# Kernel tuning notes

Measured on AMD Instinct MI355X. Metric: run time of the kernel, lower is better.

Reference implementation:

```python
import jax, jax.numpy as jnp
import numpy as np

N = 8192          # total genes
B = 16            # number of ragged batch groups (equal-size here: 512 each)
D = 768           # hidden_dim
NEG = -1.0e9      # mask fill value used by the original module


def setup_inputs() -> dict:
    key = jax.random.key(0)
    ks = jax.random.split(key, 10)
    s = 0.02
    inp = {
        "gene_embeddings": jax.random.normal(ks[0], (N, D), dtype=jnp.float32),
        # sorted group ids: 16 contiguous groups of 512 genes
        "batch": (jnp.arange(N) // (N // B)).astype(jnp.int64),
        "Wq": jax.random.normal(ks[1], (D, D), dtype=jnp.float32) * s,
        "bq": jnp.zeros((D,), dtype=jnp.float32),
        "Wk": jax.random.normal(ks[2], (D, D), dtype=jnp.float32) * s,
        "bk": jnp.zeros((D,), dtype=jnp.float32),
        "Wv": jax.random.normal(ks[3], (D, D), dtype=jnp.float32) * s,
        "bv": jnp.zeros((D,), dtype=jnp.float32),
        "Wo": jax.random.normal(ks[4], (D, D), dtype=jnp.float32) * s,
        "bo": jnp.zeros((D,), dtype=jnp.float32),
        "beta": jnp.ones((1,), dtype=jnp.float32) * 0.1,
    }
    return inp


def reference(gene_embeddings, batch, Wq, bq, Wk, bk, Wv, bv, Wo, bo, beta):
    # Single-head attention over full hidden_dim (num_heads unused in original).
    x = gene_embeddings
    q = x @ Wq.T + bq                      # [N, D]
    k = x @ Wk.T + bk
    v = x @ Wv.T + bv
    scale = 1.0 / jnp.sqrt(jnp.asarray(D, dtype=x.dtype))
    scores = (q @ k.T) * scale             # [N, N]
    # block-diagonal group mask + diagonal self-mask (same -1e9 fill as torch code)
    same_group = batch[:, None] == batch[None, :]
    eye = jnp.eye(N, dtype=bool)
    allow = same_group & (~eye)
    scores = jnp.where(allow, scores, NEG)
    weights = jax.nn.softmax(scores, axis=-1)   # dropout in eval mode -> identity
    dyn = weights @ v                       # [N, D]
    dyn = dyn @ Wo.T + bo
    return x + beta * dyn
```

## Files before the change

### kernel.cpp

```cpp
#include <hip/hip_runtime.h>
#include <hip/hip_bf16.h>
#include <cstdint>

using u16 = unsigned short;
using u32 = unsigned int;

typedef __bf16 bf16x8 __attribute__((ext_vector_type(8)));
typedef float  f32x4  __attribute__((ext_vector_type(4)));

__device__ __forceinline__ u32 f2b2(float a, float b) {
    __hip_bfloat162 h = __float22bfloat162_rn(float2{a, b});
    u32 u;
    __builtin_memcpy(&u, &h, 4);
    return u;
}
__device__ __forceinline__ float b2f(u16 b) {
    u32 u = (u32)b << 16;
    float f;
    __builtin_memcpy(&f, &u, 4);
    return f;
}

__device__ __forceinline__ void gload_lds16(const u16* g, u16* l) {
    __builtin_amdgcn_global_load_lds(
        (const __attribute__((address_space(1))) void*)g,
        (__attribute__((address_space(3))) void*)l,
        16, 0, 0);
}

__launch_bounds__(256)
__global__ void pack_kernel(const float* __restrict__ x,
                            const float* __restrict__ Wq,
                            const float* __restrict__ Wk,
                            const float* __restrict__ Wv,
                            const float* __restrict__ Wo,
                            const float* __restrict__ bq,
                            const float* __restrict__ bk,
                            const float* __restrict__ bv,
                            u16* __restrict__ xb,
                            u16* __restrict__ Wqkvb,
                            u16* __restrict__ Wob,
                            float* __restrict__ bqkv)
{
    int c = blockIdx.x * 256 + threadIdx.x;
    long e = (long)c * 8;
    const float* src; u16* dst; long off;
    if (e < 6291456L)      { src = x;  dst = xb;              off = e; }
    else if (e < 6881280L) { src = Wq; dst = Wqkvb;           off = e - 6291456L; }
    else if (e < 7471104L) { src = Wk; dst = Wqkvb + 589824;  off = e - 6881280L; }
    else if (e < 8060928L) { src = Wv; dst = Wqkvb + 1179648; off = e - 7471104L; }
    else                   { src = Wo; dst = Wob;             off = e - 8060928L; }
    float4 v0 = *(const float4*)(src + off);
    float4 v1 = *(const float4*)(src + off + 4);
    uint4 o;
    o.x = f2b2(v0.x, v0.y); o.y = f2b2(v0.z, v0.w);
    o.z = f2b2(v1.x, v1.y); o.w = f2b2(v1.z, v1.w);
    *(uint4*)(dst + off) = o;
    if (c < 768)        bqkv[c] = bq[c];
    else if (c < 1536)  bqkv[c] = bk[c - 768];
    else if (c < 2304)  bqkv[c] = bv[c - 1536];
}

template<int TM, int TN, int MODE>
__device__ __forceinline__ void gemm_body(
        const u16* __restrict__ A, int lda, long sAz,
        const u16* __restrict__ B, int ldb, long sBz,
        void* __restrict__ Cv, int ldc, long sCz,
        int K,
        const float* __restrict__ bias,
        const u16* __restrict__ xres,
        const float* __restrict__ betaPtr,
        float scale,
        u16* __restrict__ vTout)
{
    constexpr int FI = TM / 32;
    constexpr int FJ = TN / 32;
    constexpr int CA = TM / 64;
    constexpr int CB = TN / 64;

    __shared__ u16 As[2][TM * 32];
    __shared__ u16 Bs[2][TN * 32];

    const int tid  = threadIdx.x;
    const int g    = blockIdx.z;
    const u16* Ab = A + (long)g * sAz + (long)blockIdx.y * TM * lda;
    const u16* Bb = B + (long)g * sBz + (long)blockIdx.x * TN * ldb;

    const int wave = tid >> 6, lane = tid & 63;
    const int wm = (wave >> 1) * (TM / 2), wn = (wave & 1) * (TN / 2);
    const int ln15 = lane & 15, lq = lane >> 4;

    f32x4 acc[FI][FJ];
#pragma unroll
    for (int i = 0; i < FI; i++)
#pragma unroll
        for (int j = 0; j < FJ; j++)
            acc[i][j] = (f32x4){0.f, 0.f, 0.f, 0.f};

    const int srow = lane >> 2;
    const int sc   = ((lane & 3) ^ ((lane >> 4) & 3)) * 8;
    const u16* Ag[CA]; const u16* Bg[CB];
    int Al[CA], Bl[CB];
#pragma unroll
    for (int t = 0; t < CA; t++) {
        int c = wave * CA + t;
        Ag[t] = Ab + (long)(c * 16 + srow) * lda + sc;
        Al[t] = c * 512;
    }
#pragma unroll
    for (int t = 0; t < CB; t++) {
        int c = wave * CB + t;
        Bg[t] = Bb + (long)(c * 16 + srow) * ldb + sc;
        Bl[t] = c * 512;
    }

    const int foff = ln15 * 32 + ((lq ^ (ln15 >> 2)) * 8);

    const int nk = K >> 5;

#pragma unroll
    for (int t = 0; t < CA; t++) gload_lds16(Ag[t], &As[0][Al[t]]);
#pragma unroll
    for (int t = 0; t < CB; t++) gload_lds16(Bg[t], &Bs[0][Bl[t]]);

    for (int kt = 0; kt < nk; kt++) {
        const int cur = kt & 1;
        __syncthreads();
        if (kt + 1 < nk) {
            const int k0 = (kt + 1) * 32, nxt = cur ^ 1;
#pragma unroll
            for (int t = 0; t < CA; t++) gload_lds16(Ag[t] + k0, &As[nxt][Al[t]]);
#pragma unroll
            for (int t = 0; t < CB; t++) gload_lds16(Bg[t] + k0, &Bs[nxt][Bl[t]]);
        }

        bf16x8 af[FI], bfr[FJ];
#pragma unroll
        for (int i = 0; i < FI; i++)
            af[i] = *(const bf16x8*)&As[cur][(wm / 16 + i) * 512 + foff];
#pragma unroll
        for (int j = 0; j < FJ; j++)
            bfr[j] = *(const bf16x8*)&Bs[cur][(wn / 16 + j) * 512 + foff];
#pragma unroll
        for (int i = 0; i < FI; i++)
#pragma unroll
            for (int j = 0; j < FJ; j++)
                acc[i][j] = __builtin_amdgcn_mfma_f32_16x16x32_bf16(af[i], bfr[j], acc[i][j], 0, 0, 0);
    }

    const int baseRow = blockIdx.y * TM + wm;
    const int baseCol = blockIdx.x * TN + wn;

    if constexpr (MODE == 0) {
        if (baseCol < 1536) {
            u16* C = (u16*)Cv;
#pragma unroll
            for (int i = 0; i < FI; i++)
#pragma unroll
                for (int j = 0; j < FJ; j++) {
                    int col = baseCol + j * 16 + ln15;
                    float bb = bias[col];
                    u32 p01 = f2b2(acc[i][j][0] + bb, acc[i][j][1] + bb);
                    u32 p23 = f2b2(acc[i][j][2] + bb, acc[i][j][3] + bb);
                    long r0 = (long)(baseRow + i * 16 + lq * 4) * ldc + col;
                    C[r0]           = (u16)p01;
                    C[r0 + ldc]     = (u16)(p01 >> 16);
                    C[r0 + 2 * ldc] = (u16)p23;
                    C[r0 + 3 * ldc] = (u16)(p23 >> 16);
                }
        } else {
#pragma unroll
            for (int i = 0; i < FI; i++)
#pragma unroll
                for (int j = 0; j < FJ; j++) {
                    int col = baseCol + j * 16 + ln15;
                    float bb = bias[col];
                    uint2 o;
                    o.x = f2b2(acc[i][j][0] + bb, acc[i][j][1] + bb);
                    o.y = f2b2(acc[i][j][2] + bb, acc[i][j][3] + bb);
                    *(uint2*)(vTout + (long)(col - 1536) * 8192
                              + baseRow + i * 16 + lq * 4) = o;
                }
        }
    } else if constexpr (MODE == 5) {
        u16* C = (u16*)Cv + (long)g * sCz;
#pragma unroll
        for (int i = 0; i < FI; i++)
#pragma unroll
            for (int j = 0; j < FJ; j++) {
                int col = baseCol + j * 16 + ln15;
                float v[4];
#pragma unroll
                for (int r = 0; r < 4; r++) {
                    int row = baseRow + i * 16 + lq * 4 + r;
                    v[r] = acc[i][j][r] * scale;
                    if (row == col) v[r] = -1.0e9f;
                }
                u32 p01 = f2b2(v[0], v[1]);
                u32 p23 = f2b2(v[2], v[3]);
                long r0 = (long)(baseRow + i * 16 + lq * 4) * ldc + col;
                C[r0]           = (u16)p01;
                C[r0 + ldc]     = (u16)(p01 >> 16);
                C[r0 + 2 * ldc] = (u16)p23;
                C[r0 + 3 * ldc] = (u16)(p23 >> 16);
            }
    } else {
        float* C = (float*)Cv;
        float bet = betaPtr[0];
#pragma unroll
        for (int i = 0; i < FI; i++)
#pragma unroll
            for (int j = 0; j < FJ; j++)
#pragma unroll
                for (int r = 0; r < 4; r++) {
                    int row = baseRow + i * 16 + lq * 4 + r;
                    int col = baseCol + j * 16 + ln15;
                    float v = b2f(xres[(long)row * ldc + col])
                              + bet * (acc[i][j][r] + bias[col]);
                    C[(long)row * ldc + col] = v;
                }
    }
}

__launch_bounds__(256)
__global__ void k_qkv(const u16* A, const u16* B, void* C, const float* bias,
                      u16* vTout)
{
    gemm_body<128, 128, 0>(A, 768, 0, B, 768, 0, C, 1536, 0, 768,
                           bias, nullptr, nullptr, 0.f, vTout);
}
__launch_bounds__(256)
__global__ void k_scores(const u16* A, const u16* B, void* C, float scale)
{
    gemm_body<64, 128, 5>(A, 1536, 512L * 1536, B, 1536, 512L * 1536,
                          C, 512, 512L * 512, 768,
                          nullptr, nullptr, nullptr, scale, nullptr);
}
__launch_bounds__(256)
__global__ void k_out(const u16* A, const u16* B, void* C, const float* bias,
                      const u16* xres, const float* betaPtr)
{
    gemm_body<64, 128, 4>(A, 768, 0, B, 768, 0, C, 768, 0, 768,
                          bias, xres, betaPtr, 0.f, nullptr);
}

__launch_bounds__(256)
__global__ void k_pvfused(const u16* __restrict__ S,
                          const u16* __restrict__ vT,
                          u16* __restrict__ dyn)
{
    __shared__ u16 Pl[32 * 512];
    __shared__ u16 Vs[2][128 * 32];

    const int ct = blockIdx.x, rt = blockIdx.y, g = blockIdx.z;
    const int tid = threadIdx.x;
    const int wave = tid >> 6, lane = tid & 63;
    const int ln15 = lane & 15, lq = lane >> 4;

    const int srow = lane >> 2;
    const int sc   = ((lane & 3) ^ ((lane >> 4) & 3)) * 8;
    const u16* Bg[2]; int Bl[2];
#pragma unroll
    for (int t = 0; t < 2; t++) {
        int c = wave * 2 + t;
        Bg[t] = vT + (long)(ct * 128 + c * 16 + srow) * 8192 + g * 512 + sc;
        Bl[t] = c * 512;
    }
    gload_lds16(Bg[0], &Vs[0][Bl[0]]);
    gload_lds16(Bg[1], &Vs[0][Bl[1]]);

    const int r   = tid >> 3;
    const int seg = tid & 7;
    const u16* Srow = S + (long)g * 262144 + (long)(rt * 32 + r) * 512 + seg * 64;
    float e[64];
    float m = -3.0e38f;
#pragma unroll
    for (int j = 0; j < 8; j++) {
        uint4 q = *(const uint4*)(Srow + j * 8);
        u32 w[4] = {q.x, q.y, q.z, q.w};
#pragma unroll
        for (int h = 0; h < 4; h++) {
            float lo = b2f((u16)w[h]);
            float hi = b2f((u16)(w[h] >> 16));
            e[j * 8 + h * 2]     = lo;
            e[j * 8 + h * 2 + 1] = hi;
            m = fmaxf(m, fmaxf(lo, hi));
        }
    }
    m = fmaxf(m, __shfl_xor(m, 1));
    m = fmaxf(m, __shfl_xor(m, 2));
    m = fmaxf(m, __shfl_xor(m, 4));
    float sum = 0.f;
#pragma unroll
    for (int j = 0; j < 64; j++) { e[j] = __expf(e[j] - m); sum += e[j]; }
    sum += __shfl_xor(sum, 1);
    sum += __shfl_xor(sum, 2);
    sum += __shfl_xor(sum, 4);
    const float inv = 1.0f / sum;
#pragma unroll
    for (int jj = 0; jj < 8; jj++) {
        uint4 o;
        o.x = f2b2(e[jj * 8 + 0] * inv, e[jj * 8 + 1] * inv);
        o.y = f2b2(e[jj * 8 + 2] * inv, e[jj * 8 + 3] * inv);
        o.z = f2b2(e[jj * 8 + 4] * inv, e[jj * 8 + 5] * inv);
        o.w = f2b2(e[jj * 8 + 6] * inv, e[jj * 8 + 7] * inv);
        int c = seg * 8 + jj;
        *(uint4*)&Pl[(r * 64 + (c ^ (r & 7))) * 8] = o;
    }

    const int wm = (wave >> 1) * 16;
    const int wn = (wave & 1) * 64;
    const int foff = ln15 * 32 + ((lq ^ (ln15 >> 2)) * 8);
    const int prow = wm + ln15;

    f32x4 acc[4];
#pragma unroll
    for (int j = 0; j < 4; j++) acc[j] = (f32x4){0.f, 0.f, 0.f, 0.f};

    for (int kt = 0; kt < 16; kt++) {
        const int cur = kt & 1;
        __syncthreads();
        if (kt + 1 < 16) {
            const int k0 = (kt + 1) * 32, nxt = cur ^ 1;
            gload_lds16(Bg[0] + k0, &Vs[nxt][Bl[0]]);
            gload_lds16(Bg[1] + k0, &Vs[nxt][Bl[1]]);
        }
        bf16x8 ap = *(const bf16x8*)&Pl[(prow * 64 + ((kt * 4 + lq) ^ (prow & 7))) * 8];
        bf16x8 bfr[4];
#pragma unroll
        for (int j = 0; j < 4; j++)
            bfr[j] = *(const bf16x8*)&Vs[cur][(wn / 16 + j) * 512 + foff];
#pragma unroll
        for (int j = 0; j < 4; j++)
            acc[j] = __builtin_amdgcn_mfma_f32_16x16x32_bf16(ap, bfr[j], acc[j], 0, 0, 0);
    }

    u16* D = dyn + (long)(g * 512 + rt * 32 + wm + lq * 4) * 768;
#pragma unroll
    for (int j = 0; j < 4; j++) {
        int col = ct * 128 + wn + j * 16 + ln15;
        u32 p01 = f2b2(acc[j][0], acc[j][1]);
        u32 p23 = f2b2(acc[j][2], acc[j][3]);
        D[col]            = (u16)p01;
        D[col + 768]      = (u16)(p01 >> 16);
        D[col + 2 * 768]  = (u16)p23;
        D[col + 3 * 768]  = (u16)(p23 >> 16);
    }
}

extern "C" void kernel_launch(void* const* d_in, const int* in_sizes, int n_in,
                              void* d_out, int out_size, void* d_ws, size_t ws_size,
                              hipStream_t stream)
{
    const float* x    = (const float*)d_in[0];
    const float* Wq   = (const float*)d_in[2];
    const float* bq   = (const float*)d_in[3];
    const float* Wk   = (const float*)d_in[4];
    const float* bk   = (const float*)d_in[5];
    const float* Wv   = (const float*)d_in[6];
    const float* bv   = (const float*)d_in[7];
    const float* Wo   = (const float*)d_in[8];
    const float* bo   = (const float*)d_in[9];
    const float* beta = (const float*)d_in[10];
    float* out = (float*)d_out;

    char* ws = (char*)d_ws;
    u16*   qk    = (u16*)(ws + 0);
    u16*   dyn   = (u16*)(ws + 0);
    u16*   vT    = (u16*)(ws + 25165824);
    u16*   xb    = (u16*)(ws + 37748736);
    u16*   S     = (u16*)(ws + 50331648);
    u16*   Wqkvb = (u16*)(ws + 58720256);
    u16*   Wob   = (u16*)(ws + 62259200);
    float* bqkv  = (float*)(ws + 63438848);

    const float scale = 0.03608439182435161f;

    pack_kernel<<<4224, 256, 0, stream>>>(x, Wq, Wk, Wv, Wo, bq, bk, bv,
                                          xb, Wqkvb, Wob, bqkv);

    k_qkv<<<dim3(18, 64, 1), 256, 0, stream>>>(xb, Wqkvb, (void*)qk, bqkv, vT);

    k_scores<<<dim3(4, 8, 16), 256, 0, stream>>>(qk, qk + 768, (void*)S, scale);

    k_pvfused<<<dim3(6, 16, 16), 256, 0, stream>>>(S, vT, dyn);

    k_out<<<dim3(6, 128, 1), 256, 0, stream>>>(dyn, Wob, (void*)out, bo, xb, beta);
}
```

Measured before the change: 224.0 us.

## Fold output projection into value projection to drop the final GEMM

Precomputes Wo·Wv as a combined matrix and Wo·bv+bo as a combined bias, so the value projection produces already-projected values. The PV kernel then writes the residual output directly, which removes the separate output-projection GEMM over all 8192 rows and the dyn intermediate round trip. In exchange it adds a small 768x768 weight GEMM and a transpose in the pack step. The product weight is rounded to bf16, which slightly changes numerics.

```diff
diff --git a/kernel.cpp b/kernel.cpp
--- a/kernel.cpp
+++ b/kernel.cpp
@@ -37,28 +37,68 @@
                             const float* __restrict__ bq,
                             const float* __restrict__ bk,
                             const float* __restrict__ bv,
+                            const float* __restrict__ bo,
                             u16* __restrict__ xb,
                             u16* __restrict__ Wqkvb,
                             u16* __restrict__ Wob,
-                            float* __restrict__ bqkv)
-{
-    int c = blockIdx.x * 256 + threadIdx.x;
-    long e = (long)c * 8;
-    const float* src; u16* dst; long off;
-    if (e < 6291456L)      { src = x;  dst = xb;              off = e; }
-    else if (e < 6881280L) { src = Wq; dst = Wqkvb;           off = e - 6291456L; }
-    else if (e < 7471104L) { src = Wk; dst = Wqkvb + 589824;  off = e - 6881280L; }
-    else if (e < 8060928L) { src = Wv; dst = Wqkvb + 1179648; off = e - 7471104L; }
-    else                   { src = Wo; dst = Wob;             off = e - 8060928L; }
-    float4 v0 = *(const float4*)(src + off);
-    float4 v1 = *(const float4*)(src + off + 4);
-    uint4 o;
-    o.x = f2b2(v0.x, v0.y); o.y = f2b2(v0.z, v0.w);
-    o.z = f2b2(v1.x, v1.y); o.w = f2b2(v1.z, v1.w);
-    *(uint4*)(dst + off) = o;
-    if (c < 768)        bqkv[c] = bq[c];
-    else if (c < 1536)  bqkv[c] = bk[c - 768];
-    else if (c < 2304)  bqkv[c] = bv[c - 1536];
+                            u16* __restrict__ WvTb,
+                            float* __restrict__ bqk,
+                            float* __restrict__ bvoo)
+{
+    __shared__ u16 tl[64][72];
+    const int b = blockIdx.x, tid = threadIdx.x;
+
+    if (b < 3936) {
+        int c = b * 256 + tid;
+        long e = (long)c * 8;
+        const float* src; u16* dst; long off;
+        if (e < 6291456L)      { src = x;  dst = xb;             off = e; }
+        else if (e < 6881280L) { src = Wq; dst = Wqkvb;          off = e - 6291456L; }
+        else if (e < 7471104L) { src = Wk; dst = Wqkvb + 589824; off = e - 6881280L; }
+        else                   { src = Wo; dst = Wob;            off = e - 7471104L; }
+        float4 v0 = *(const float4*)(src + off);
+        float4 v1 = *(const float4*)(src + off + 4);
+        uint4 o;
+        o.x = f2b2(v0.x, v0.y); o.y = f2b2(v0.z, v0.w);
+        o.z = f2b2(v1.x, v1.y); o.w = f2b2(v1.z, v1.w);
+        *(uint4*)(dst + off) = o;
+        if (c < 768)       bqk[c] = bq[c];
+        else if (c < 1536) bqk[c] = bk[c - 768];
+    } else if (b < 4080) {
+        int t = b - 3936;
+        int tr = t / 12, tc = t % 12;
+        int lr = tid >> 2, lcb = (tid & 3) * 16;
+        const float* src = Wv + (long)(tr * 64 + lr) * 768 + tc * 64 + lcb;
+#pragma unroll
+        for (int q = 0; q < 4; q++) {
+            float4 v = *(const float4*)(src + q * 4);
+            u32 p0 = f2b2(v.x, v.y), p1 = f2b2(v.z, v.w);
+            tl[lr][lcb + q * 4 + 0] = (u16)p0;
+            tl[lr][lcb + q * 4 + 1] = (u16)(p0 >> 16);
+            tl[lr][lcb + q * 4 + 2] = (u16)p1;
+            tl[lr][lcb + q * 4 + 3] = (u16)(p1 >> 16);
+        }
+        __syncthreads();
+        int li = tid >> 2, lkb = (tid & 3) * 16;
+        u16 o[16];
+#pragma unroll
+        for (int j = 0; j < 16; j++) o[j] = tl[lkb + j][li];
+        u16* dst = WvTb + (long)(tc * 64 + li) * 768 + tr * 64 + lkb;
+#pragma unroll
+        for (int j = 0; j < 16; j++) dst[j] = o[j];
+    } else {
+        int wave = tid >> 6, lane = tid & 63;
+        int j = (b - 4080) * 4 + wave;
+        float acc = 0.f;
+#pragma unroll
+        for (int i = 0; i < 12; i++) {
+            int k = i * 64 + lane;
+            acc += Wo[(long)j * 768 + k] * bv[k];
+        }
+#pragma unroll
+        for (int d = 32; d; d >>= 1) acc += __shfl_xor(acc, d);
+        if (lane == 0) bvoo[j] = acc + bo[j];
+    }
 }
 
 template<int TM, int TN, int MODE>
@@ -68,8 +108,6 @@
         void* __restrict__ Cv, int ldc, long sCz,
         int K,
         const float* __restrict__ bias,
-        const u16* __restrict__ xres,
-        const float* __restrict__ betaPtr,
         float scale,
         u16* __restrict__ vTout)
 {
@@ -115,7 +153,6 @@
     }
 
     const int foff = ln15 * 32 + ((lq ^ (ln15 >> 2)) * 8);
-
     const int nk = K >> 5;
 
 #pragma unroll
@@ -174,10 +211,9 @@
 #pragma unroll
                 for (int j = 0; j < FJ; j++) {
                     int col = baseCol + j * 16 + ln15;
-                    float bb = bias[col];
                     uint2 o;
-                    o.x = f2b2(acc[i][j][0] + bb, acc[i][j][1] + bb);
-                    o.y = f2b2(acc[i][j][2] + bb, acc[i][j][3] + bb);
+                    o.x = f2b2(acc[i][j][0], acc[i][j][1]);
+                    o.y = f2b2(acc[i][j][2], acc[i][j][3]);
                     *(uint2*)(vTout + (long)(col - 1536) * 8192
                               + baseRow + i * 16 + lq * 4) = o;
                 }
@@ -205,49 +241,51 @@
                 C[r0 + 3 * ldc] = (u16)(p23 >> 16);
             }
     } else {
-        float* C = (float*)Cv;
-        float bet = betaPtr[0];
+        u16* C = (u16*)Cv;
 #pragma unroll
         for (int i = 0; i < FI; i++)
 #pragma unroll
-            for (int j = 0; j < FJ; j++)
-#pragma unroll
-                for (int r = 0; r < 4; r++) {
-                    int row = baseRow + i * 16 + lq * 4 + r;
-                    int col = baseCol + j * 16 + ln15;
-                    float v = b2f(xres[(long)row * ldc + col])
-                              + bet * (acc[i][j][r] + bias[col]);
-                    C[(long)row * ldc + col] = v;
-                }
-    }
-}
-
+            for (int j = 0; j < FJ; j++) {
+                int col = baseCol + j * 16 + ln15;
+                u32 p01 = f2b2(acc[i][j][0], acc[i][j][1]);
+                u32 p23 = f2b2(acc[i][j][2], acc[i][j][3]);
+                long r0 = (long)(baseRow + i * 16 + lq * 4) * ldc + col;
+                C[r0]           = (u16)p01;
+                C[r0 + ldc]     = (u16)(p01 >> 16);
+                C[r0 + 2 * ldc] = (u16)p23;
+                C[r0 + 3 * ldc] = (u16)(p23 >> 16);
+            }
+    }
+}
+
+__launch_bounds__(256)
+__global__ void k_wvo(const u16* A, const u16* B, void* C)
+{
+    gemm_body<64, 128, 3>(A, 768, 0, B, 768, 0, C, 768, 0, 768,
+                          nullptr, 0.f, nullptr);
+}
 __launch_bounds__(256)
 __global__ void k_qkv(const u16* A, const u16* B, void* C, const float* bias,
                       u16* vTout)
 {
     gemm_body<128, 128, 0>(A, 768, 0, B, 768, 0, C, 1536, 0, 768,
-                           bias, nullptr, nullptr, 0.f, vTout);
+                           bias, 0.f, vTout);
 }
 __launch_bounds__(256)
 __global__ void k_scores(const u16* A, const u16* B, void* C, float scale)
 {
     gemm_body<64, 128, 5>(A, 1536, 512L * 1536, B, 1536, 512L * 1536,
                           C, 512, 512L * 512, 768,
-                          nullptr, nullptr, nullptr, scale, nullptr);
-}
+                          nullptr, scale, nullptr);
+}
+
 __launch_bounds__(256)
-__global__ void k_out(const u16* A, const u16* B, void* C, const float* bias,
-                      const u16* xres, const float* betaPtr)
-{
-    gemm_body<64, 128, 4>(A, 768, 0, B, 768, 0, C, 768, 0, 768,
-                          bias, xres, betaPtr, 0.f, nullptr);
-}
-
-__launch_bounds__(256)
-__global__ void k_pvfused(const u16* __restrict__ S,
-                          const u16* __restrict__ vT,
-                          u16* __restrict__ dyn)
+__global__ void k_pvwfused(const u16* __restrict__ S,
+                           const u16* __restrict__ vwT,
+                           const u16* __restrict__ xb,
+                           float* __restrict__ out,
+                           const float* __restrict__ bvoo,
+                           const float* __restrict__ betaPtr)
 {
     __shared__ u16 Pl[32 * 512];
     __shared__ u16 Vs[2][128 * 32];
@@ -263,7 +301,7 @@
 #pragma unroll
     for (int t = 0; t < 2; t++) {
         int c = wave * 2 + t;
-        Bg[t] = vT + (long)(ct * 128 + c * 16 + srow) * 8192 + g * 512 + sc;
+        Bg[t] = vwT + (long)(ct * 128 + c * 16 + srow) * 8192 + g * 512 + sc;
         Bl[t] = c * 512;
     }
     gload_lds16(Bg[0], &Vs[0][Bl[0]]);
@@ -335,16 +373,18 @@
             acc[j] = __builtin_amdgcn_mfma_f32_16x16x32_bf16(ap, bfr[j], acc[j], 0, 0, 0);
     }
 
-    u16* D = dyn + (long)(g * 512 + rt * 32 + wm + lq * 4) * 768;
+    const float bet = betaPtr[0];
+    const long rowBase = (long)(g * 512 + rt * 32 + wm + lq * 4);
+    const u16* Xr = xb + rowBase * 768;
+    float* O = out + rowBase * 768;
 #pragma unroll
     for (int j = 0; j < 4; j++) {
         int col = ct * 128 + wn + j * 16 + ln15;
-        u32 p01 = f2b2(acc[j][0], acc[j][1]);
-        u32 p23 = f2b2(acc[j][2], acc[j][3]);
-        D[col]            = (u16)p01;
-        D[col + 768]      = (u16)(p01 >> 16);
-        D[col + 2 * 768]  = (u16)p23;
-        D[col + 3 * 768]  = (u16)(p23 >> 16);
+        float bb = bvoo[col];
+#pragma unroll
+        for (int rr = 0; rr < 4; rr++)
+            O[rr * 768 + col] = b2f(Xr[rr * 768 + col])
+                                + bet * (acc[j][rr] + bb);
     }
 }
 
@@ -366,24 +406,26 @@
 
     char* ws = (char*)d_ws;
     u16*   qk    = (u16*)(ws + 0);
-    u16*   dyn   = (u16*)(ws + 0);
-    u16*   vT    = (u16*)(ws + 25165824);
+    u16*   vwT   = (u16*)(ws + 25165824);
     u16*   xb    = (u16*)(ws + 37748736);
     u16*   S     = (u16*)(ws + 50331648);
     u16*   Wqkvb = (u16*)(ws + 58720256);
     u16*   Wob   = (u16*)(ws + 62259200);
-    float* bqkv  = (float*)(ws + 63438848);
+    u16*   WvTb  = (u16*)(ws + 63438848);
+    float* bqk   = (float*)(ws + 64618496);
+    float* bvoo  = (float*)(ws + 64624640);
 
     const float scale = 0.03608439182435161f;
 
-    pack_kernel<<<4224, 256, 0, stream>>>(x, Wq, Wk, Wv, Wo, bq, bk, bv,
-                                          xb, Wqkvb, Wob, bqkv);
-
-    k_qkv<<<dim3(18, 64, 1), 256, 0, stream>>>(xb, Wqkvb, (void*)qk, bqkv, vT);
+    pack_kernel<<<4272, 256, 0, stream>>>(x, Wq, Wk, Wv, Wo, bq, bk, bv, bo,
+                                          xb, Wqkvb, Wob, WvTb, bqk, bvoo);
+
+    k_wvo<<<dim3(6, 12, 1), 256, 0, stream>>>(Wob, WvTb,
+                                              (void*)(Wqkvb + 1536L * 768));
+
+    k_qkv<<<dim3(18, 64, 1), 256, 0, stream>>>(xb, Wqkvb, (void*)qk, bqk, vwT);
 
     k_scores<<<dim3(4, 8, 16), 256, 0, stream>>>(qk, qk + 768, (void*)S, scale);
 
-    k_pvfused<<<dim3(6, 16, 16), 256, 0, stream>>>(S, vT, dyn);
-
-    k_out<<<dim3(6, 128, 1), 256, 0, stream>>>(dyn, Wob, (void*)out, bo, xb, beta);
-}
+    k_pvwfused<<<dim3(6, 16, 16), 256, 0, stream>>>(S, vwT, xb, out, bvoo, beta);
+}
```

Measured after the change: 213.5 us. -4.7%, faster.
